# Optimization experiments

Hardware: AMD Instinct MI355X
Metric: run time of the kernel (lower is better)

## Reference

```python
import jax, jax.numpy as jnp
import numpy as np
import math

D_MODEL = 1024
RANK = 128
K_RANK = 128
N_KNOW = 32768
COARSE_K = 64
FINE_K = 16
B, S = 2, 2048


def setup_inputs() -> dict:
    key = jax.random.key(0)
    ks = jax.random.split(key, 6)
    x = jax.random.normal(ks[0], (B, S, D_MODEL), dtype=jnp.float32)
    h = jax.random.normal(ks[1], (B, S, RANK), dtype=jnp.float32)
    W_router = jax.random.normal(ks[2], (D_MODEL, N_KNOW), dtype=jnp.float32) * 0.02
    W_q = jax.random.normal(ks[3], (K_RANK, RANK), dtype=jnp.float32) * 0.02  # Linear(rank->k_rank) weight
    K_all = jax.random.normal(ks[4], (N_KNOW, K_RANK), dtype=jnp.float32) * 0.02
    V_all = jax.random.normal(ks[5], (N_KNOW, D_MODEL), dtype=jnp.float32) * 0.02
    return {"x": x, "h": h, "W_router": W_router, "W_q": W_q, "K_all": K_all, "V_all": V_all}


def reference(x, h, W_router, W_q, K_all, V_all):
    # Stage 1: coarse candidate selection via router logits
    k_logits = jnp.einsum('bsd,dn->bsn', x, W_router)              # [B,S,N]
    coarse_scores, candidate_idx = jax.lax.top_k(k_logits, COARSE_K)  # [B,S,Ck]

    # Stage 2: fine matching with compressed query
    query = jnp.einsum('bsr,kr->bsk', h, W_q)                      # [B,S,K_RANK]
    K_cand = K_all[candidate_idx]                                  # [B,S,Ck,K_RANK] gather
    fine_scores = jnp.einsum('bsd,bscd->bsc', query, K_cand) / math.sqrt(K_RANK)
    fine_topk_scores, fine_local_idx = jax.lax.top_k(fine_scores, FINE_K)  # [B,S,Fk]
    fine_weights = jax.nn.softmax(fine_topk_scores, axis=-1)
    fine_global_idx = jnp.take_along_axis(candidate_idx, fine_local_idx, axis=-1)  # [B,S,Fk]

    selected_V = V_all[fine_global_idx]                            # [B,S,Fk,D] gather
    output = jnp.einsum('bsfd,bsf->bsd', selected_V, fine_weights)  # weighted combine
    return output
```

## Files before the change

### kernel.cpp

```cpp
#include <hip/hip_runtime.h>
#include <cstdint>

#define D_MODEL 1024
#define RANK 128
#define K_RANK_ 128
#define N_KNOW 32768
#define COARSE_K 64
#define FINE_K 16
#define NTOK 4096
#define MSEL 96
#define DELTA 1.3e-3f
#define SC 4096

using u32 = unsigned int;
using u64 = unsigned long long;
typedef _Float16 half8 __attribute__((ext_vector_type(8)));
typedef __attribute__((ext_vector_type(4))) float f32x4;

__device__ __forceinline__ u32 ordf(float v) {
    u32 u = __float_as_uint(v);
    return (u & 0x80000000u) ? ~u : (u | 0x80000000u);
}
__device__ __forceinline__ float unordf(u32 o) {
    return (o & 0x80000000u) ? __uint_as_float(o ^ 0x80000000u)
                             : __uint_as_float(~o);
}
__device__ __forceinline__ ushort f2h(float f) {
    union { _Float16 h; ushort u; } cv; cv.h = (_Float16)f; return cv.u;
}
__device__ __forceinline__ float h2f(ushort u) {
    union { ushort u; _Float16 h; } cv; cv.u = u; return (float)cv.h;
}
__device__ __forceinline__ void gload16(const void* g, void* l) {
    __builtin_amdgcn_global_load_lds(
        (const __attribute__((address_space(1))) char*)g,
        (__attribute__((address_space(3))) char*)l, 16, 0, 0);
}

__global__ __launch_bounds__(256)
void kcvt_x(const float* __restrict__ in, ushort* __restrict__ xh)
{
    int i = blockIdx.x * 256 + threadIdx.x;
    float4 v = ((const float4*)in)[i];
    ((ushort4*)xh)[i] = make_ushort4(f2h(v.x), f2h(v.y), f2h(v.z), f2h(v.w));
}

__global__ __launch_bounds__(256)
void kcvt_wt(const float* __restrict__ W, ushort* __restrict__ out, int col0)
{
    __shared__ float tile[32][33];
    const int nb = blockIdx.x * 32;
    const int kb = blockIdx.y * 32;
    const int tx = threadIdx.x & 31, ty = threadIdx.x >> 5;
#pragma unroll
    for (int q = 0; q < 4; ++q)
        tile[ty + q * 8][tx] = W[(size_t)(kb + ty + q * 8) * N_KNOW + col0 + nb + tx];
    __syncthreads();
#pragma unroll
    for (int q = 0; q < 4; ++q) {
        float v = tile[tx][ty + q * 8];
        out[(size_t)(nb + ty + q * 8) * D_MODEL + kb + tx] = f2h(v);
    }
}

__global__ __launch_bounds__(512, 2)
void k1f8(const ushort* __restrict__ xh, const ushort* __restrict__ wt,
          ushort* __restrict__ L)
{
    __shared__ ushort lds[2][32768];

    const int tid = threadIdx.x;
    const int nwg = gridDim.x;
    int wfl = blockIdx.x;
    wfl = (wfl & 7) * (nwg >> 3) + (wfl >> 3);
    const int bm = (wfl & 15) * 256;
    const int bn = (wfl >> 4) * 256;

    const int lane = tid & 63;
    const int wid = tid >> 6;
    const int wm = wid >> 2, wn = wid & 3;
    const int lr = lane & 15, g = lane >> 4;

    const ushort* gA[4]; const ushort* gB[4];
#pragma unroll
    for (int i = 0; i < 4; ++i) {
        const int o = i * 512 + tid;
        const int row = o >> 3;
        const int gslot = (o & 7) ^ (row & 7);
        gA[i] = xh + (size_t)(bm + row) * D_MODEL + gslot * 8;
        gB[i] = wt + (size_t)(bn + row) * D_MODEL + gslot * 8;
    }

    int aoff[2][8], boff[2][4];
#pragma unroll
    for (int ks = 0; ks < 2; ++ks) {
#pragma unroll
        for (int mf = 0; mf < 8; ++mf) {
            int row = wm * 128 + mf * 16 + lr;
            aoff[ks][mf] = row * 128 + (((ks * 4 + g) ^ (row & 7)) << 4);
        }
#pragma unroll
        for (int nf = 0; nf < 4; ++nf) {
            int row = wn * 64 + nf * 16 + lr;
            boff[ks][nf] = 32768 + row * 128 + (((ks * 4 + g) ^ (row & 7)) << 4);
        }
    }

    f32x4 acc[8][4];
#pragma unroll
    for (int mf = 0; mf < 8; ++mf)
#pragma unroll
        for (int nf = 0; nf < 4; ++nf) acc[mf][nf] = (f32x4)(0.f);

#define SAH(b, t, h)                                                           \
    {                                                                          \
        gload16(gA[2*(h)]   + (t) * 64,                                        \
                (char*)&lds[(b)][0] + ((2*(h)) * 512 + tid) * 16);             \
        gload16(gA[2*(h)+1] + (t) * 64,                                        \
                (char*)&lds[(b)][0] + ((2*(h)+1) * 512 + tid) * 16);           \
    }
#define SBH(b, t, h)                                                           \
    {                                                                          \
        gload16(gB[2*(h)]   + (t) * 64,                                        \
                (char*)&lds[(b)][0] + 32768 + ((2*(h)) * 512 + tid) * 16);     \
        gload16(gB[2*(h)+1] + (t) * 64,                                        \
                (char*)&lds[(b)][0] + 32768 + ((2*(h)+1) * 512 + tid) * 16);   \
    }

#define LDA4(lb, ks, base)                                                     \
    a0 = *(const half8*)((lb) + aoff[ks][(base) + 0]);                         \
    a1 = *(const half8*)((lb) + aoff[ks][(base) + 1]);                         \
    a2 = *(const half8*)((lb) + aoff[ks][(base) + 2]);                         \
    a3 = *(const half8*)((lb) + aoff[ks][(base) + 3]);

#define LDB4(lb, ks, bb)                                                       \
    bb[0] = *(const half8*)((lb) + boff[ks][0]);                               \
    bb[1] = *(const half8*)((lb) + boff[ks][1]);                               \
    bb[2] = *(const half8*)((lb) + boff[ks][2]);                               \
    bb[3] = *(const half8*)((lb) + boff[ks][3]);

#define MFMA16(mbase, bb)                                                      \
    __builtin_amdgcn_s_setprio(1);                                             \
    _Pragma("unroll")                                                          \
    for (int nf = 0; nf < 4; ++nf) {                                           \
        acc[(mbase)+0][nf] = __builtin_amdgcn_mfma_f32_16x16x32_f16(           \
            a0, bb[nf], acc[(mbase)+0][nf], 0, 0, 0);                          \
        acc[(mbase)+1][nf] = __builtin_amdgcn_mfma_f32_16x16x32_f16(           \
            a1, bb[nf], acc[(mbase)+1][nf], 0, 0, 0);                          \
        acc[(mbase)+2][nf] = __builtin_amdgcn_mfma_f32_16x16x32_f16(           \
            a2, bb[nf], acc[(mbase)+2][nf], 0, 0, 0);                          \
        acc[(mbase)+3][nf] = __builtin_amdgcn_mfma_f32_16x16x32_f16(           \
            a3, bb[nf], acc[(mbase)+3][nf], 0, 0, 0);                          \
    }                                                                          \
    __builtin_amdgcn_s_setprio(0);

#define SBAR()                                                                 \
    __builtin_amdgcn_sched_barrier(0);                                         \
    __builtin_amdgcn_s_barrier();                                              \
    __builtin_amdgcn_sched_barrier(0);

    SBH(0, 0, 0); SBH(0, 0, 1);
    SAH(0, 0, 0); SAH(0, 0, 1);
    SBH(1, 1, 0); SBH(1, 1, 1);

    const char* lb0 = (const char*)&lds[0][0];
    const char* lb1 = (const char*)&lds[1][0];
    half8 b0q[4], b1q[4];

    for (int i = 0; i < 8; ++i) {
        const int t1 = 2 * i + 1;
        const int tn0 = 2 * i + 2, tn1 = 2 * i + 3;
        const bool st = tn0 < 16;
        half8 a0, a1, a2, a3;

        asm volatile("s_waitcnt vmcnt(4)" ::: "memory");
        SBAR();
        LDA4(lb0, 0, 0);
        LDB4(lb0, 0, b0q);
        SAH(1, t1, 0);
        MFMA16(0, b0q);
        LDA4(lb0, 1, 0);
        LDB4(lb0, 1, b1q);
        SAH(1, t1, 1);
        MFMA16(0, b1q);
        SBAR();
        LDA4(lb0, 0, 4);
        if (st) SBH(0, tn0, 0);
        MFMA16(4, b0q);
        LDA4(lb0, 1, 4);
        if (st) SBH(0, tn0, 1);
        MFMA16(4, b1q);
        if (i < 7) asm volatile("s_waitcnt vmcnt(4)" ::: "memory");
        else       asm volatile("s_waitcnt vmcnt(0)" ::: "memory");
        SBAR();
        LDA4(lb1, 0, 0);
        LDB4(lb1, 0, b0q);
        if (st) SAH(0, tn0, 0);
        MFMA16(0, b0q);
        LDA4(lb1, 1, 0);
        LDB4(lb1, 1, b1q);
        if (st) SAH(0, tn0, 1);
        MFMA16(0, b1q);
        SBAR();
        LDA4(lb1, 0, 4);
        if (st) SBH(1, tn1, 0);
        MFMA16(4, b0q);
        LDA4(lb1, 1, 4);
        if (st) SBH(1, tn1, 1);
        MFMA16(4, b1q);
    }
#undef SAH
#undef SBH
#undef LDA4
#undef LDB4
#undef MFMA16
#undef SBAR

    const int crow0 = bm + wm * 128 + g * 4;
    const int ccol  = bn + wn * 64 + lr;
#pragma unroll
    for (int mf = 0; mf < 8; ++mf)
#pragma unroll
        for (int nf = 0; nf < 4; ++nf)
#pragma unroll
            for (int r = 0; r < 4; ++r)
                L[(size_t)(crow0 + mf * 16 + r) * SC + ccol + nf * 16] =
                    f2h(acc[mf][nf][r]);
}

template <int M>
__global__ __launch_bounds__(256)
void k2_topk(const ushort* __restrict__ L, u64* __restrict__ R,
             int col0, int stripe)
{
    const int tt = blockIdx.x;
    const int tid = threadIdx.x;

    __shared__ u64 buf[4224];
    __shared__ int scnt;
    __shared__ int sred[4];

    u64 key[16];
    const uint4* row8 = (const uint4*)(L + (size_t)tt * SC);
#pragma unroll
    for (int q = 0; q < 2; ++q) {
        uint4 v = row8[q * 256 + tid];
        const int c = col0 + (q * 256 + tid) * 8;
        u32 wv[4] = {v.x, v.y, v.z, v.w};
#pragma unroll
        for (int d = 0; d < 4; ++d) {
            float f0 = h2f((ushort)(wv[d] & 0xFFFFu));
            float f1 = h2f((ushort)(wv[d] >> 16));
            key[q * 8 + d * 2]     = ((u64)ordf(f0) << 32) | (u32)(N_KNOW - 1 - (c + d * 2));
            key[q * 8 + d * 2 + 1] = ((u64)ordf(f1) << 32) | (u32)(N_KNOW - 2 - (c + d * 2));
        }
    }

    u64 tkey;
    if (stripe == 0) {
        u32 lo = 0, hi = 0xFFFFFFFFu;
        for (int it = 0; it < 28; ++it) {
            if (hi - lo <= 1) break;
            u32 mid = lo + ((hi - lo) >> 1);
            int c = 0;
#pragma unroll
            for (int j = 0; j < 16; ++j) c += ((u32)(key[j] >> 32) > mid) ? 1 : 0;
#pragma unroll
            for (int o = 32; o; o >>= 1) c += __shfl_xor(c, o);
            if ((tid & 63) == 0) sred[tid >> 6] = c;
            __syncthreads();
            c = sred[0] + sred[1] + sred[2] + sred[3];
            __syncthreads();
            if (c >= M) { lo = mid; if (c <= 768) break; }
            else hi = mid;
        }
        tkey = ((u64)lo << 32) | 0xFFFFFFFFull;
        if (tid == 0) scnt = 0;
    } else {
        tkey = R[(size_t)tt * M + (M - 1)];
        if (tid < M) buf[tid] = R[(size_t)tt * M + tid];
        if (tid == 0) scnt = M;
    }
    __syncthreads();

#pragma unroll
    for (int j = 0; j < 16; ++j)
        if (key[j] > tkey) {
            int p = atomicAdd(&scnt, 1);
            if (p < 4224) buf[p] = key[j];
        }
    __syncthreads();

    const int n = min(scnt, 4224);
    for (int i = tid; i < n; i += 256) {
        u64 ki = buf[i];
        int r = 0;
        for (int j = 0; j < n; ++j) r += (buf[j] > ki) ? 1 : 0;
        if (r < M) R[(size_t)tt * M + r] = ki;
    }
}

__global__ __launch_bounds__(256)
void k2b_band(const u64* __restrict__ R96, u32* __restrict__ jobs,
              int* __restrict__ jobCount, u32* __restrict__ band)
{
    __shared__ float sv[4][MSEL];
    const int tid = threadIdx.x;
    const int w = tid >> 6, lane = tid & 63;
    const int tt = blockIdx.x * 4 + w;

    sv[w][lane] = unordf((u32)(R96[(size_t)tt * MSEL + lane] >> 32));
    if (lane < MSEL - 64)
        sv[w][lane + 64] = unordf((u32)(R96[(size_t)tt * MSEL + lane + 64] >> 32));
    __syncthreads();

    const float t = sv[w][COARSE_K - 1];
    int cg = 0, cl = 0;
    for (int j = lane; j < MSEL; j += 64) {
        cg += (sv[w][j] > t + DELTA) ? 1 : 0;
        cl += (sv[w][j] < t - DELTA) ? 1 : 0;
    }
#pragma unroll
    for (int o = 32; o; o >>= 1) { cg += __shfl_xor(cg, o); cl += __shfl_xor(cl, o); }

    int lo = cg, hi = MSEL - 1 - cl;
    if (lo > COARSE_K - 1) lo = COARSE_K - 1;
    if (hi < COARSE_K - 1) hi = COARSE_K - 1;

    u32 b;
    if (lo == COARSE_K - 1 && hi == COARSE_K - 1) {
        b = 0x80000000u | 63u | (63u << 8);
    } else {
        int nj = hi - lo + 1;
        int base = 0;
        if (lane == 0) base = atomicAdd(jobCount, nj);
        base = __shfl(base, 0);
        for (int k = lane; k < nj; k += 64)
            jobs[base + k] = ((u32)tt << 8) | (u32)(lo + k);
        b = (u32)lo | ((u32)hi << 8);
    }
    if (lane == 0) band[tt] = b;
}

__global__ __launch_bounds__(256)
void k2b_exec(const u32* __restrict__ jobs, const int* __restrict__ jobCount,
              const u64* __restrict__ R96, const float* __restrict__ x,
              const float* __restrict__ W, u64* __restrict__ nk)
{
    __shared__ float red[4];
    const int tid = threadIdx.x;
    const int n = *jobCount;
    for (int j = blockIdx.x; j < n; j += gridDim.x) {
        u32 jd = jobs[j];
        int tt = jd >> 8, idx = jd & 255;
        u64 key = R96[(size_t)tt * MSEL + idx];
        int col = (N_KNOW - 1) - (int)(u32)(key & 0xFFFFFFFFu);
        float p = 0.f;
#pragma unroll
        for (int q = 0; q < 4; ++q) {
            int k = tid + q * 256;
            p = fmaf(x[(size_t)tt * D_MODEL + k], W[(size_t)k * N_KNOW + col], p);
        }
#pragma unroll
        for (int o = 32; o; o >>= 1) p += __shfl_xor(p, o);
        if ((tid & 63) == 0) red[tid >> 6] = p;
        __syncthreads();
        if (tid == 0) {
            float e = red[0] + red[1] + red[2] + red[3];
            nk[(size_t)tt * MSEL + idx] = ((u64)ordf(e) << 32) | (key & 0xFFFFFFFFu);
        }
        __syncthreads();
    }
}

__global__ __launch_bounds__(128)
void k2b_final(const u64* __restrict__ R96, const u64* __restrict__ nk,
               const u32* __restrict__ band, u64* __restrict__ R64)
{
    const int tt = blockIdx.x;
    const int tid = threadIdx.x;
    __shared__ u64 keys[MSEL];
    __shared__ u64 nkk[MSEL];

    const u32 b = band[tt];
    if (tid < MSEL) keys[tid] = R96[(size_t)tt * MSEL + tid];
    const int lo = b & 0xFF, hi = (b >> 8) & 0xFF;
    const bool trivial = (b & 0x80000000u) != 0;
    if (!trivial && tid >= lo && tid <= hi && tid < MSEL)
        nkk[tid] = nk[(size_t)tt * MSEL + tid];
    __syncthreads();

    if (trivial) {
        if (tid < COARSE_K) R64[(size_t)tt * COARSE_K + tid] = keys[tid];
        return;
    }
    if (tid < lo) R64[(size_t)tt * COARSE_K + tid] = keys[tid];
    const int mwin = COARSE_K - lo;
    if (tid >= lo && tid <= hi) {
        u64 me = nkk[tid];
        int r = 0;
        for (int j = lo; j <= hi; ++j) r += (nkk[j] > me) ? 1 : 0;
        if (r < mwin) R64[(size_t)tt * COARSE_K + lo + r] = keys[tid];
    }
}

__device__ __forceinline__ void fma4(float4& a, float w, const float4& v) {
    a.x = fmaf(w, v.x, a.x); a.y = fmaf(w, v.y, a.y);
    a.z = fmaf(w, v.z, a.z); a.w = fmaf(w, v.w, a.w);
}

__global__ __launch_bounds__(256)
void k3f(const float* __restrict__ h, const float* __restrict__ Wq,
         const float* __restrict__ Kall, const u64* __restrict__ R,
         int* __restrict__ fidx, float* __restrict__ fw)
{
    __shared__ float hq[4][RANK];
    __shared__ float qv[4][K_RANK_];

    const int tid = threadIdx.x;
    const int w = tid >> 6, lane = tid & 63;
    const int tt = blockIdx.x * 4 + w;

    {
        float2 hv = *(const float2*)(h + (size_t)tt * RANK + lane * 2);
        hq[w][lane * 2] = hv.x;
        hq[w][lane * 2 + 1] = hv.y;
    }
    const u64 key = R[(size_t)tt * COARSE_K + lane];
    const int ci = (N_KNOW - 1) - (int)(u32)(key & 0xFFFFFFFFu);
    __syncthreads();

    {
        float s0 = 0.f, s1 = 0.f;
        const float4* w0 = (const float4*)(Wq + (size_t)(lane * 2) * RANK);
        const float4* w1 = (const float4*)(Wq + (size_t)(lane * 2 + 1) * RANK);
#pragma unroll
        for (int r4 = 0; r4 < RANK / 4; ++r4) {
            float4 a = w0[r4], b = w1[r4];
            const float* hh = &hq[w][r4 * 4];
            s0 = fmaf(a.x, hh[0], s0); s0 = fmaf(a.y, hh[1], s0);
            s0 = fmaf(a.z, hh[2], s0); s0 = fmaf(a.w, hh[3], s0);
            s1 = fmaf(b.x, hh[0], s1); s1 = fmaf(b.y, hh[1], s1);
            s1 = fmaf(b.z, hh[2], s1); s1 = fmaf(b.w, hh[3], s1);
        }
        qv[w][lane * 2] = s0;
        qv[w][lane * 2 + 1] = s1;
    }
    __syncthreads();

    float sc;
    {
        float s = 0.f;
        const float4* kr = (const float4*)(Kall + (size_t)ci * K_RANK_);
#pragma unroll
        for (int r4 = 0; r4 < K_RANK_ / 4; ++r4) {
            float4 a = kr[r4];
            const float* qq = &qv[w][r4 * 4];
            s = fmaf(a.x, qq[0], s); s = fmaf(a.y, qq[1], s);
            s = fmaf(a.z, qq[2], s); s = fmaf(a.w, qq[3], s);
        }
        sc = s * 0.08838834764831845f;
    }

    const u64 myk = ((u64)ordf(sc) << 32) | (u32)(63 - lane);
    int rnk = 0;
#pragma unroll
    for (int j = 0; j < 64; ++j) {
        u64 kj = __shfl(myk, j);
        rnk += (kj > myk) ? 1 : 0;
    }

    float smax = sc;
#pragma unroll
    for (int o = 32; o; o >>= 1) smax = fmaxf(smax, __shfl_xor(smax, o));
    float e = (rnk < FINE_K) ? expf(sc - smax) : 0.f;
    float esum = e;
#pragma unroll
    for (int o = 32; o; o >>= 1) esum += __shfl_xor(esum, o);
    if (rnk < FINE_K) {
        fidx[(size_t)tt * FINE_K + rnk] = ci;
        fw[(size_t)tt * FINE_K + rnk] = e / esum;
    }
}

__global__ __launch_bounds__(256)
void k3g(const int* __restrict__ fidx, const float* __restrict__ fw,
         const float* __restrict__ Vall, float* __restrict__ out)
{
    __shared__ int si[FINE_K];
    __shared__ float sw[FINE_K];
    const int tt = blockIdx.x;
    const int tid = threadIdx.x;
    if (tid < FINE_K) {
        si[tid] = fidx[(size_t)tt * FINE_K + tid];
        sw[tid] = fw[(size_t)tt * FINE_K + tid];
    }
    __syncthreads();

    float4 a = make_float4(0.f, 0.f, 0.f, 0.f);
#pragma unroll
    for (int f = 0; f < FINE_K; ++f) {
        const float4 v = *(const float4*)(Vall + (size_t)si[f] * D_MODEL + tid * 4);
        fma4(a, sw[f], v);
    }
    ((float4*)(out + (size_t)tt * D_MODEL))[tid] = a;
}

extern "C" void kernel_launch(void* const* d_in, const int* in_sizes, int n_in,
                              void* d_out, int out_size, void* d_ws, size_t ws_size,
                              hipStream_t stream)
{
    const float* x  = (const float*)d_in[0];
    const float* h  = (const float*)d_in[1];
    const float* Wr = (const float*)d_in[2];
    const float* Wq = (const float*)d_in[3];
    const float* Ka = (const float*)d_in[4];
    const float* Va = (const float*)d_in[5];
    float* out = (float*)d_out;

    const size_t fixed =
        (size_t)NTOK * D_MODEL * 2 +
        (size_t)NTOK * SC * 2 +
        (size_t)NTOK * MSEL * 8 * 2 +
        (size_t)NTOK * COARSE_K * 8 +
        (size_t)NTOK * MSEL * 4 +
        4096 +
        (size_t)NTOK * 4 +
        (size_t)NTOK * FINE_K * 8;

    int WCH = N_KNOW;
    while (WCH > SC && fixed + (size_t)WCH * D_MODEL * 2 > ws_size)
        WCH >>= 1;

    char* p = (char*)d_ws;
    ushort* wt   = (ushort*)p;  p += (size_t)WCH * D_MODEL * 2;
    ushort* xh   = (ushort*)p;  p += (size_t)NTOK * D_MODEL * 2;
    ushort* Lh   = (ushort*)p;  p += (size_t)NTOK * SC * 2;
    u64*    R96  = (u64*)p;     p += (size_t)NTOK * MSEL * 8;
    u64*    nk   = (u64*)p;     p += (size_t)NTOK * MSEL * 8;
    u64*    R64  = (u64*)p;     p += (size_t)NTOK * COARSE_K * 8;
    u32*    jobs = (u32*)p;     p += (size_t)NTOK * MSEL * 4;
    int*    jobCount = (int*)p; p += 4096;
    u32*    band = (u32*)p;     p += (size_t)NTOK * 4;
    int*    fidx = (int*)p;     p += (size_t)NTOK * FINE_K * 4;
    float*  fw   = (float*)p;   p += (size_t)NTOK * FINE_K * 4;

    hipMemsetAsync(jobCount, 0, 4, stream);

    kcvt_x<<<NTOK * D_MODEL / 4 / 256, 256, 0, stream>>>(x, xh);

    const int nstripe = N_KNOW / SC;
    const int spc = WCH / SC;
    for (int s = 0; s < nstripe; ++s) {
        if (s % spc == 0)
            kcvt_wt<<<dim3(WCH / 32, D_MODEL / 32), 256, 0, stream>>>(Wr, wt, s * SC);
        const ushort* wts = wt + (size_t)((s % spc) * SC) * D_MODEL;
        k1f8<<<(SC / 256) * (NTOK / 256), 512, 0, stream>>>(xh, wts, Lh);
        k2_topk<MSEL><<<NTOK, 256, 0, stream>>>(Lh, R96, s * SC, s);
    }

    k2b_band<<<NTOK / 4, 256, 0, stream>>>(R96, jobs, jobCount, band);
    k2b_exec<<<8192, 256, 0, stream>>>(jobs, jobCount, R96, x, Wr, nk);
    k2b_final<<<NTOK, 128, 0, stream>>>(R96, nk, band, R64);

    k3f<<<NTOK / 4, 256, 0, stream>>>(h, Wq, Ka, R64, fidx, fw);
    k3g<<<NTOK, 256, 0, stream>>>(fidx, fw, Va, out);
}
```

Baseline: 813.1 us.

## Double the router logit stripe width and process two halves per top-k block

Widens the stripe of router logits written to the intermediate buffer from 4096 to 8192 columns, so the per-stripe top-k kernel handles twice as many candidates per launch, in two halves. This halves the number of stripe passes and kernel launches and the repeated merge against the running top-M list. The threshold is derived from the first half only, so the candidate buffer may hold more entries (capped at 4224), which could make the quadratic rank step more expensive. The larger staging buffer also doubles its memory footprint.

Result: slower. 831.4 us (+2.2%).

```diff
diff --git a/kernel.cpp b/kernel.cpp
--- a/kernel.cpp
+++ b/kernel.cpp
@@ -10,7 +10,7 @@
 #define NTOK 4096
 #define MSEL 96
 #define DELTA 1.3e-3f
-#define SC 4096
+#define SC 8192
 
 using u32 = unsigned int;
 using u64 = unsigned long long;
@@ -240,24 +240,35 @@
     __shared__ int scnt;
     __shared__ int sred[4];
 
+    const uint4* row8 = (const uint4*)(L + (size_t)tt * SC);
     u64 key[16];
-    const uint4* row8 = (const uint4*)(L + (size_t)tt * SC);
-#pragma unroll
-    for (int q = 0; q < 2; ++q) {
-        uint4 v = row8[q * 256 + tid];
-        const int c = col0 + (q * 256 + tid) * 8;
-        u32 wv[4] = {v.x, v.y, v.z, v.w};
-#pragma unroll
-        for (int d = 0; d < 4; ++d) {
-            float f0 = h2f((ushort)(wv[d] & 0xFFFFu));
-            float f1 = h2f((ushort)(wv[d] >> 16));
-            key[q * 8 + d * 2]     = ((u64)ordf(f0) << 32) | (u32)(N_KNOW - 1 - (c + d * 2));
-            key[q * 8 + d * 2 + 1] = ((u64)ordf(f1) << 32) | (u32)(N_KNOW - 2 - (c + d * 2));
-        }
-    }
+
+#define LOADKEYS(half)                                                         \
+    _Pragma("unroll")                                                          \
+    for (int q = 0; q < 2; ++q) {                                              \
+        uint4 v = row8[(half) * 512 + q * 256 + tid];                          \
+        const int c = col0 + (half) * 4096 + (q * 256 + tid) * 8;              \
+        u32 wv[4] = {v.x, v.y, v.z, v.w};                                      \
+        _Pragma("unroll")                                                      \
+        for (int d = 0; d < 4; ++d) {                                          \
+            float f0 = h2f((ushort)(wv[d] & 0xFFFFu));                         \
+            float f1 = h2f((ushort)(wv[d] >> 16));                             \
+            key[q * 8 + d * 2]     = ((u64)ordf(f0) << 32) | (u32)(N_KNOW - 1 - (c + d * 2)); \
+            key[q * 8 + d * 2 + 1] = ((u64)ordf(f1) << 32) | (u32)(N_KNOW - 2 - (c + d * 2)); \
+        }                                                                      \
+    }
+
+#define FILTERKEYS()                                                           \
+    _Pragma("unroll")                                                          \
+    for (int j = 0; j < 16; ++j)                                               \
+        if (key[j] > tkey) {                                                   \
+            int p = atomicAdd(&scnt, 1);                                       \
+            if (p < 4224) buf[p] = key[j];                                     \
+        }
 
     u64 tkey;
     if (stripe == 0) {
+        LOADKEYS(0);
         u32 lo = 0, hi = 0xFFFFFFFFu;
         for (int it = 0; it < 28; ++it) {
             if (hi - lo <= 1) break;
@@ -276,20 +287,23 @@
         }
         tkey = ((u64)lo << 32) | 0xFFFFFFFFull;
         if (tid == 0) scnt = 0;
+        __syncthreads();
+        FILTERKEYS();
+        LOADKEYS(1);
+        FILTERKEYS();
     } else {
         tkey = R[(size_t)tt * M + (M - 1)];
         if (tid < M) buf[tid] = R[(size_t)tt * M + tid];
         if (tid == 0) scnt = M;
-    }
-    __syncthreads();
-
-#pragma unroll
-    for (int j = 0; j < 16; ++j)
-        if (key[j] > tkey) {
-            int p = atomicAdd(&scnt, 1);
-            if (p < 4224) buf[p] = key[j];
-        }
-    __syncthreads();
+        __syncthreads();
+        LOADKEYS(0);
+        FILTERKEYS();
+        LOADKEYS(1);
+        FILTERKEYS();
+    }
+    __syncthreads();
+#undef LOADKEYS
+#undef FILTERKEYS
 
     const int n = min(scnt, 4224);
     for (int i = tid; i < n; i += 256) {
```
